# Kernel tuning notes

Measured on AMD Instinct MI355X. Metric: run time of the kernel, lower is better.

The kernel has to match this reference:

```python
import jax, jax.numpy as jnp
import numpy as np

N = 50000   # nodes
E = 800000  # edges (avg degree 16)
D = 96      # feature dim (in = hidden = out)


def setup_inputs() -> dict:
    key = jax.random.key(0)
    ks = jax.random.split(key, 6)
    scale = 1.0 / np.sqrt(D)
    return {
        "x": jax.random.normal(ks[0], (N, D), jnp.float32),
        "edge_index": jax.random.randint(ks[1], (2, E), 0, N, dtype=jnp.int64),
        "W1": jax.random.normal(ks[2], (D, D), jnp.float32) * scale,
        "b1": jnp.zeros((D,), jnp.float32),
        "a1": jnp.full((1,), 0.25, jnp.float32),  # PReLU weight
        "W2": jax.random.normal(ks[3], (D, D), jnp.float32) * scale,
        "b2": jnp.zeros((D,), jnp.float32),
    }


def _gcn_conv(x, W, b, src, dst, norm, n):
    # GCNConv: linear transform, then degree-normalized scatter-add aggregation
    h = x @ W                               # [N, D_out]
    msg = h[src] * norm[:, None]            # gather + scale, [E+N, D_out]
    out = jax.ops.segment_sum(msg, dst, num_segments=n)
    return out + b


def reference(x, edge_index, W1, b1, a1, W2, b2):
    n = x.shape[0]
    # add self loops (PyG gcn_norm default, fill_value=1.0)
    loop = jnp.arange(n, dtype=edge_index.dtype)
    src = jnp.concatenate([edge_index[0], loop])
    dst = jnp.concatenate([edge_index[1], loop])
    # symmetric normalization: D^{-1/2} A D^{-1/2}
    ones = jnp.ones(src.shape[0], dtype=x.dtype)
    deg = jax.ops.segment_sum(ones, dst, num_segments=n)
    dinv = jnp.where(deg > 0, jax.lax.rsqrt(deg), 0.0)
    norm = dinv[src] * dinv[dst]

    h = _gcn_conv(x, W1, b1, src, dst, norm, n)
    h = jnp.where(h > 0, h, a1 * h)  # PReLU (dropout p=0.0 is a no-op)
    h = _gcn_conv(h, W2, b2, src, dst, norm, n)
    return h
```

## Files before the change

### kernel.cpp

```cpp
#include <hip/hip_runtime.h>
#include <hip/hip_bf16.h>

#define NNODES 50000
#define NEDGES 800000
#define DIM    96
#define NBUCK  196
#define CAP    4608
#define TM     64
#define XPAD   104
#define PCH    3125

typedef __attribute__((ext_vector_type(8))) short   short8;
typedef __attribute__((ext_vector_type(4))) float   float4v;

__device__ __forceinline__ float loadF(const void* p, long i, int isbf) {
    return isbf ? __bfloat162float(((const __hip_bfloat16*)p)[i])
                : ((const float*)p)[i];
}
__device__ __forceinline__ int clampN(int v) {
    return v < 0 ? 0 : (v >= NNODES ? NNODES - 1 : v);
}
__device__ __forceinline__ int edgeDst(const int* w, int e, int is64) {
    return clampN(is64 ? w[2 * (NEDGES + e)] : w[NEDGES + e]);
}
__device__ __forceinline__ int edgeSrc(const int* w, int e, int is64) {
    return clampN(is64 ? w[2 * e] : w[e]);
}

__global__ void k_sniff(const unsigned* __restrict__ xw,
                        const unsigned* __restrict__ ew,
                        int* __restrict__ flags,
                        int* __restrict__ bcur) {
    int lane = threadIdx.x;
    for (int i = lane; i < NBUCK; i += 64) bcur[i] = 0;
    int bad = 0, nz = 0;
    for (int r = 0; r < 4; ++r) {
        unsigned w  = xw[lane + 64 * r];
        unsigned lo = w & 0xffffu;
        unsigned ex = (lo >> 7) & 0xffu;
        if (!(lo == 0u || (ex >= 90u && ex <= 145u))) bad++;
        unsigned o = ew[2 * (lane + 64 * r) + 1];
        if (o != 0u) nz++;
    }
    for (int off = 32; off; off >>= 1) {
        bad += __shfl_down(bad, off);
        nz  += __shfl_down(nz,  off);
    }
    if (lane == 0) {
        flags[0] = (bad <= 32) ? 1 : 0;
        flags[1] = (nz  <  4) ? 1 : 0;
    }
}

__global__ __launch_bounds__(256) void k_part(const int* __restrict__ w,
                                              int* __restrict__ bcur,
                                              unsigned* __restrict__ ebuf,
                                              const int* __restrict__ flags) {
    __shared__ unsigned pack[PCH];
    __shared__ int h[NBUCK];
    __shared__ int base[NBUCK];
    const int is64 = flags[1];
    const int tid  = threadIdx.x;
    const int e0   = blockIdx.x * PCH;

    for (int i = tid; i < NBUCK; i += 256) h[i] = 0;
    __syncthreads();
    for (int k = tid; k < PCH; k += 256) {
        int e = e0 + k;
        int s = edgeSrc(w, e, is64);
        int d = edgeDst(w, e, is64);
        pack[k] = ((unsigned)d << 16) | (unsigned)s;
        atomicAdd(&h[d >> 8], 1);
    }
    __syncthreads();
    for (int i = tid; i < NBUCK; i += 256) {
        int c = h[i];
        base[i] = c ? i * CAP + atomicAdd(&bcur[i], c) : 0;
        h[i] = 0;
    }
    __syncthreads();
    for (int k = tid; k < PCH; k += 256) {
        unsigned r = pack[k];
        int b = r >> 24;
        int pos = base[b] + atomicAdd(&h[b], 1);
        if (pos < (b + 1) * CAP) ebuf[pos] = r;
    }
}

__global__ __launch_bounds__(512) void k_csr(const unsigned* __restrict__ ebuf,
                                             const int* __restrict__ bcur,
                                             int* __restrict__ rowbeg,
                                             int* __restrict__ rowend,
                                             unsigned short* __restrict__ col,
                                             float* __restrict__ dinv) {
    __shared__ int h256[256];
    __shared__ int sc[256];
    __shared__ int cur[256];
    const int b   = blockIdx.x;
    const int tid = threadIdx.x;
    int cnt = bcur[b]; if (cnt > CAP) cnt = CAP;
    const int e0 = b * CAP;
    const int e1 = e0 + cnt;

    if (tid < 256) h256[tid] = 0;
    __syncthreads();
    for (int e = e0 + tid; e < e1; e += 512)
        atomicAdd(&h256[(ebuf[e] >> 16) & 255], 1);
    __syncthreads();
    int v = 0;
    if (tid < 256) { v = h256[tid]; sc[tid] = v; }
    __syncthreads();
    for (int off = 1; off < 256; off <<= 1) {
        int t2 = 0;
        if (tid < 256 && tid >= off) t2 = sc[tid - off];
        __syncthreads();
        if (tid < 256) sc[tid] += t2;
        __syncthreads();
    }
    if (tid < 256) {
        int start = e0 + sc[tid] - v;
        cur[tid] = start;
        int node = b * 256 + tid;
        if (node < NNODES) {
            rowbeg[node] = start;
            rowend[node] = start + v;
            dinv[node] = rsqrtf((float)v + 1.0f);
        }
    }
    __syncthreads();
    for (int e = e0 + tid; e < e1; e += 512) {
        unsigned r = ebuf[e];
        int pos = atomicAdd(&cur[(r >> 16) & 255], 1);
        col[pos] = (unsigned short)(r & 0xffffu);
    }
}

__global__ __launch_bounds__(256) void k_gemm_mfma(
        const void* __restrict__ X, int x_force_bf16,
        const void* __restrict__ W,
        const float* __restrict__ dinv,
        __hip_bfloat16* __restrict__ g,
        const int* __restrict__ flags) {
    __shared__ __hip_bfloat16 Xs[TM * XPAD];
    __shared__ __hip_bfloat16 Wt[DIM * XPAD];

    const int t    = threadIdx.x;
    const int fbf  = flags[0];
    const int xbf  = x_force_bf16 ? 1 : fbf;
    const int row0 = blockIdx.x * TM;

    if (!fbf) {
        const float4* Wv = (const float4*)W;
        for (int idx = t; idx < DIM * DIM / 4; idx += 256) {
            int k = idx / (DIM / 4);
            int n = (idx - k * (DIM / 4)) * 4;
            float4 w4 = Wv[idx];
            Wt[(n + 0) * XPAD + k] = __float2bfloat16(w4.x);
            Wt[(n + 1) * XPAD + k] = __float2bfloat16(w4.y);
            Wt[(n + 2) * XPAD + k] = __float2bfloat16(w4.z);
            Wt[(n + 3) * XPAD + k] = __float2bfloat16(w4.w);
        }
    } else {
        for (int idx = t; idx < DIM * DIM; idx += 256) {
            int k = idx / DIM, n = idx - k * DIM;
            Wt[n * XPAD + k] = __float2bfloat16(loadF(W, idx, 1));
        }
    }
    if (!xbf) {
        const float4* Xv = (const float4*)X;
        for (int idx = t; idx < TM * (DIM / 4); idx += 256) {
            int r = idx / (DIM / 4);
            int c = (idx - r * (DIM / 4)) * 4;
            int gr = row0 + r;
            float4 vv = {0.f, 0.f, 0.f, 0.f};
            if (gr < NNODES) vv = Xv[(size_t)gr * (DIM / 4) + (c >> 2)];
            *(__hip_bfloat162*)&Xs[r * XPAD + c] =
                __halves2bfloat162(__float2bfloat16(vv.x), __float2bfloat16(vv.y));
            *(__hip_bfloat162*)&Xs[r * XPAD + c + 2] =
                __halves2bfloat162(__float2bfloat16(vv.z), __float2bfloat16(vv.w));
        }
    } else {
        const short* Xs16 = (const short*)X;
        for (int idx = t; idx < TM * (DIM / 8); idx += 256) {
            int r  = idx / (DIM / 8);
            int c8 = idx - r * (DIM / 8);
            int gr = row0 + r;
            short8 vv = {0, 0, 0, 0, 0, 0, 0, 0};
            if (gr < NNODES) vv = *(const short8*)(Xs16 + (size_t)gr * DIM + c8 * 8);
            *(short8*)((short*)Xs + r * XPAD + c8 * 8) = vv;
        }
    }
    __syncthreads();

    const int wave = t >> 6;
    const int lane = t & 63;
    const int m    = lane & 15;
    const int quad = lane >> 4;

    const short* xsp = (const short*)Xs;
    short8 a[3];
#pragma unroll
    for (int kt = 0; kt < 3; ++kt)
        a[kt] = *(const short8*)(xsp + (wave * 16 + m) * XPAD + kt * 32 + quad * 8);

    float dv[4];
#pragma unroll
    for (int r2 = 0; r2 < 4; ++r2) {
        int gr = row0 + wave * 16 + quad * 4 + r2;
        dv[r2] = (gr < NNODES) ? dinv[gr] : 0.f;
    }

    const short* wtp = (const short*)Wt;
#pragma unroll
    for (int nt = 0; nt < 6; ++nt) {
        float4v acc = {0.f, 0.f, 0.f, 0.f};
#pragma unroll
        for (int kt = 0; kt < 3; ++kt) {
            short8 b = *(const short8*)(wtp + (nt * 16 + m) * XPAD + kt * 32 + quad * 8);
            acc = __builtin_amdgcn_mfma_f32_16x16x32_bf16(a[kt], b, acc, 0, 0, 0);
        }
#pragma unroll
        for (int r2 = 0; r2 < 4; ++r2) {
            int gr = row0 + wave * 16 + quad * 4 + r2;
            if (gr < NNODES)
                g[(size_t)gr * DIM + nt * 16 + m] = __float2bfloat16(acc[r2] * dv[r2]);
        }
    }
}

__global__ __launch_bounds__(256) void k_aggr(
        const __hip_bfloat16* __restrict__ g,
        const int* __restrict__ rowbeg,
        const int* __restrict__ rowend,
        const unsigned short* __restrict__ col,
        const float* __restrict__ dinv,
        const void* __restrict__ b,
        const void* __restrict__ a1,
        void* __restrict__ out,
        const int* __restrict__ flags, int prelu) {
    const int wave = threadIdx.x >> 6;
    const int lane = threadIdx.x & 63;
    const int row  = blockIdx.x * 4 + wave;
    if (row >= NNODES) return;
    const int fbf = flags[0];
    const __hip_bfloat162* gv = (const __hip_bfloat162*)g;
    const int c = lane;

    float2 acc = {0.f, 0.f};
    if (c < 48) acc = __bfloat1622float2(gv[(size_t)row * 48 + c]);

    const int p0 = rowbeg[row], p1 = rowend[row];
    int i = p0;
    for (; i + 16 <= p1; i += 16) {
        int s[16];
#pragma unroll
        for (int k = 0; k < 16; ++k) s[k] = col[i + k];
        if (c < 48) {
            float2 v[16];
#pragma unroll
            for (int k = 0; k < 16; ++k)
                v[k] = __bfloat1622float2(gv[(size_t)s[k] * 48 + c]);
            float2 t0, t1, t2, t3;
            t0.x = (v[0].x + v[1].x) + (v[2].x + v[3].x);
            t0.y = (v[0].y + v[1].y) + (v[2].y + v[3].y);
            t1.x = (v[4].x + v[5].x) + (v[6].x + v[7].x);
            t1.y = (v[4].y + v[5].y) + (v[6].y + v[7].y);
            t2.x = (v[8].x + v[9].x) + (v[10].x + v[11].x);
            t2.y = (v[8].y + v[9].y) + (v[10].y + v[11].y);
            t3.x = (v[12].x + v[13].x) + (v[14].x + v[15].x);
            t3.y = (v[12].y + v[13].y) + (v[14].y + v[15].y);
            acc.x += (t0.x + t1.x) + (t2.x + t3.x);
            acc.y += (t0.y + t1.y) + (t2.y + t3.y);
        }
    }
    for (; i + 8 <= p1; i += 8) {
        int s[8];
#pragma unroll
        for (int k = 0; k < 8; ++k) s[k] = col[i + k];
        if (c < 48) {
            float2 v[8];
#pragma unroll
            for (int k = 0; k < 8; ++k)
                v[k] = __bfloat1622float2(gv[(size_t)s[k] * 48 + c]);
            acc.x += ((v[0].x + v[1].x) + (v[2].x + v[3].x))
                   + ((v[4].x + v[5].x) + (v[6].x + v[7].x));
            acc.y += ((v[0].y + v[1].y) + (v[2].y + v[3].y))
                   + ((v[4].y + v[5].y) + (v[6].y + v[7].y));
        }
    }
    for (; i + 4 <= p1; i += 4) {
        int s0 = col[i], s1 = col[i+1], s2 = col[i+2], s3 = col[i+3];
        if (c < 48) {
            float2 v0 = __bfloat1622float2(gv[(size_t)s0 * 48 + c]);
            float2 v1 = __bfloat1622float2(gv[(size_t)s1 * 48 + c]);
            float2 v2 = __bfloat1622float2(gv[(size_t)s2 * 48 + c]);
            float2 v3 = __bfloat1622float2(gv[(size_t)s3 * 48 + c]);
            acc.x += (v0.x + v1.x) + (v2.x + v3.x);
            acc.y += (v0.y + v1.y) + (v2.y + v3.y);
        }
    }
    for (; i < p1; ++i) {
        int s = col[i];
        if (c < 48) {
            float2 v = __bfloat1622float2(gv[(size_t)s * 48 + c]);
            acc.x += v.x; acc.y += v.y;
        }
    }

    if (c < 48) {
        float dv = dinv[row];
        float vx = dv * acc.x + loadF(b, 2 * c,     fbf);
        float vy = dv * acc.y + loadF(b, 2 * c + 1, fbf);
        if (prelu) {
            float alpha = loadF(a1, 0, fbf);
            vx = vx > 0.f ? vx : alpha * vx;
            vy = vy > 0.f ? vy : alpha * vy;
            ((__hip_bfloat162*)out)[(size_t)row * 48 + c] =
                __halves2bfloat162(__float2bfloat16(vx), __float2bfloat16(vy));
        } else if (fbf) {
            ((__hip_bfloat162*)out)[(size_t)row * 48 + c] =
                __halves2bfloat162(__float2bfloat16(vx), __float2bfloat16(vy));
        } else {
            float2 o; o.x = vx; o.y = vy;
            ((float2*)out)[(size_t)row * 48 + c] = o;
        }
    }
}

extern "C" void kernel_launch(void* const* d_in, const int* in_sizes, int n_in,
                              void* d_out, int out_size, void* d_ws, size_t ws_size,
                              hipStream_t stream) {
    const void* x  = d_in[0];
    const int*  ei = (const int*)d_in[1];
    const void* W1 = d_in[2];
    const void* b1 = d_in[3];
    const void* a1 = d_in[4];
    const void* W2 = d_in[5];
    const void* b2 = d_in[6];

    size_t off = 0;
    auto alloc = [&](size_t bytes) { size_t p = off; off = (off + bytes + 255) & ~(size_t)255; return p; };
    char* ws = (char*)d_ws;
    int*            flags  = (int*)           (ws + alloc(1024));
    float*          dinv   = (float*)         (ws + alloc((size_t)NNODES * 4));
    int*            bcur   = (int*)           (ws + alloc((size_t)NBUCK * 4));
    int*            rowbeg = (int*)           (ws + alloc((size_t)NNODES * 4));
    int*            rowend = (int*)           (ws + alloc((size_t)NNODES * 4));
    unsigned*       ebuf   = (unsigned*)      (ws + alloc((size_t)NBUCK * CAP * 4));
    unsigned short* col    = (unsigned short*)(ws + alloc((size_t)NBUCK * CAP * 2));
    __hip_bfloat16* g      = (__hip_bfloat16*)(ws + alloc((size_t)NNODES * DIM * 2));
    __hip_bfloat16* g2     = (__hip_bfloat16*)(ws + alloc((size_t)NNODES * DIM * 2));
    if (ws_size < off) return;

    k_sniff<<<1, 64, 0, stream>>>((const unsigned*)x, (const unsigned*)ei, flags, bcur);
    k_part <<<256, 256, 0, stream>>>(ei, bcur, ebuf, flags);
    k_csr  <<<NBUCK, 512, 0, stream>>>(ebuf, bcur, rowbeg, rowend, col, dinv);

    const int gemm_grid = (NNODES + TM - 1) / TM;
    const int aggr_grid = (NNODES + 3) / 4;

    k_gemm_mfma<<<gemm_grid, 256, 0, stream>>>(x, 0, W1, dinv, g, flags);
    k_aggr<<<aggr_grid, 256, 0, stream>>>(g, rowbeg, rowend, col, dinv, b1, a1, g2, flags, 1);

    k_gemm_mfma<<<gemm_grid, 256, 0, stream>>>(g2, 1, W2, dinv, g, flags);
    k_aggr<<<aggr_grid, 256, 0, stream>>>(g, rowbeg, rowend, col, dinv, b2, a1, d_out, flags, 0);
}
```

Before: 204.0 us.

## Replace bucketed CSR build with fixed-capacity per-row slots filled by global atomics

The two-pass bucket partition plus per-bucket CSR construction is replaced by a single scatter kernel that atomically bumps each destination's degree and writes the source into a fixed 64-slot row. dinv is recomputed from the degree on the fly, and the aggregation tail loops are merged into one masked 16-wide pass. This removes two kernels and an intermediate edge buffer. In exchange it adds contention on global atomics, makes neighbour order nondeterministic, and silently drops edges beyond 64 per node, which is only safe because random graphs with average degree 16 rarely exceed that.

```diff
diff --git a/kernel.cpp b/kernel.cpp
--- a/kernel.cpp
+++ b/kernel.cpp
@@ -4,11 +4,9 @@
 #define NNODES 50000
 #define NEDGES 800000
 #define DIM    96
-#define NBUCK  196
-#define CAP    4608
+#define RCAP   64
 #define TM     64
 #define XPAD   104
-#define PCH    3125
 
 typedef __attribute__((ext_vector_type(8))) short   short8;
 typedef __attribute__((ext_vector_type(4))) float   float4v;
@@ -20,125 +18,54 @@
 __device__ __forceinline__ int clampN(int v) {
     return v < 0 ? 0 : (v >= NNODES ? NNODES - 1 : v);
 }
-__device__ __forceinline__ int edgeDst(const int* w, int e, int is64) {
-    return clampN(is64 ? w[2 * (NEDGES + e)] : w[NEDGES + e]);
-}
-__device__ __forceinline__ int edgeSrc(const int* w, int e, int is64) {
-    return clampN(is64 ? w[2 * e] : w[e]);
-}
-
-__global__ void k_sniff(const unsigned* __restrict__ xw,
-                        const unsigned* __restrict__ ew,
-                        int* __restrict__ flags,
-                        int* __restrict__ bcur) {
-    int lane = threadIdx.x;
-    for (int i = lane; i < NBUCK; i += 64) bcur[i] = 0;
-    int bad = 0, nz = 0;
-    for (int r = 0; r < 4; ++r) {
-        unsigned w  = xw[lane + 64 * r];
+
+__global__ __launch_bounds__(256) void k_init(const unsigned* __restrict__ xw,
+                                              const unsigned* __restrict__ ew,
+                                              int* __restrict__ flags,
+                                              int* __restrict__ deg) {
+    const int t = blockIdx.x * 256 + threadIdx.x;
+    const int nth = gridDim.x * 256;
+    for (int i = t; i < NNODES; i += nth) deg[i] = 0;
+    if (blockIdx.x == 0) {
+        __shared__ int sn[2];
+        if (threadIdx.x < 2) sn[threadIdx.x] = 0;
+        __syncthreads();
+        unsigned w  = xw[threadIdx.x];
         unsigned lo = w & 0xffffu;
         unsigned ex = (lo >> 7) & 0xffu;
-        if (!(lo == 0u || (ex >= 90u && ex <= 145u))) bad++;
-        unsigned o = ew[2 * (lane + 64 * r) + 1];
-        if (o != 0u) nz++;
-    }
-    for (int off = 32; off; off >>= 1) {
-        bad += __shfl_down(bad, off);
-        nz  += __shfl_down(nz,  off);
-    }
-    if (lane == 0) {
-        flags[0] = (bad <= 32) ? 1 : 0;
-        flags[1] = (nz  <  4) ? 1 : 0;
-    }
-}
-
-__global__ __launch_bounds__(256) void k_part(const int* __restrict__ w,
-                                              int* __restrict__ bcur,
-                                              unsigned* __restrict__ ebuf,
-                                              const int* __restrict__ flags) {
-    __shared__ unsigned pack[PCH];
-    __shared__ int h[NBUCK];
-    __shared__ int base[NBUCK];
-    const int is64 = flags[1];
-    const int tid  = threadIdx.x;
-    const int e0   = blockIdx.x * PCH;
-
-    for (int i = tid; i < NBUCK; i += 256) h[i] = 0;
-    __syncthreads();
-    for (int k = tid; k < PCH; k += 256) {
-        int e = e0 + k;
-        int s = edgeSrc(w, e, is64);
-        int d = edgeDst(w, e, is64);
-        pack[k] = ((unsigned)d << 16) | (unsigned)s;
-        atomicAdd(&h[d >> 8], 1);
-    }
-    __syncthreads();
-    for (int i = tid; i < NBUCK; i += 256) {
-        int c = h[i];
-        base[i] = c ? i * CAP + atomicAdd(&bcur[i], c) : 0;
-        h[i] = 0;
-    }
-    __syncthreads();
-    for (int k = tid; k < PCH; k += 256) {
-        unsigned r = pack[k];
-        int b = r >> 24;
-        int pos = base[b] + atomicAdd(&h[b], 1);
-        if (pos < (b + 1) * CAP) ebuf[pos] = r;
-    }
-}
-
-__global__ __launch_bounds__(512) void k_csr(const unsigned* __restrict__ ebuf,
-                                             const int* __restrict__ bcur,
-                                             int* __restrict__ rowbeg,
-                                             int* __restrict__ rowend,
-                                             unsigned short* __restrict__ col,
-                                             float* __restrict__ dinv) {
-    __shared__ int h256[256];
-    __shared__ int sc[256];
-    __shared__ int cur[256];
-    const int b   = blockIdx.x;
-    const int tid = threadIdx.x;
-    int cnt = bcur[b]; if (cnt > CAP) cnt = CAP;
-    const int e0 = b * CAP;
-    const int e1 = e0 + cnt;
-
-    if (tid < 256) h256[tid] = 0;
-    __syncthreads();
-    for (int e = e0 + tid; e < e1; e += 512)
-        atomicAdd(&h256[(ebuf[e] >> 16) & 255], 1);
-    __syncthreads();
-    int v = 0;
-    if (tid < 256) { v = h256[tid]; sc[tid] = v; }
-    __syncthreads();
-    for (int off = 1; off < 256; off <<= 1) {
-        int t2 = 0;
-        if (tid < 256 && tid >= off) t2 = sc[tid - off];
+        if (!(lo == 0u || (ex >= 90u && ex <= 145u))) atomicAdd(&sn[0], 1);
+        if (ew[2 * threadIdx.x + 1] != 0u) atomicAdd(&sn[1], 1);
         __syncthreads();
-        if (tid < 256) sc[tid] += t2;
-        __syncthreads();
-    }
-    if (tid < 256) {
-        int start = e0 + sc[tid] - v;
-        cur[tid] = start;
-        int node = b * 256 + tid;
-        if (node < NNODES) {
-            rowbeg[node] = start;
-            rowend[node] = start + v;
-            dinv[node] = rsqrtf((float)v + 1.0f);
-        }
-    }
-    __syncthreads();
-    for (int e = e0 + tid; e < e1; e += 512) {
-        unsigned r = ebuf[e];
-        int pos = atomicAdd(&cur[(r >> 16) & 255], 1);
-        col[pos] = (unsigned short)(r & 0xffffu);
-    }
+        if (threadIdx.x == 0) {
+            flags[0] = (sn[0] <= 32) ? 1 : 0;
+            flags[1] = (sn[1] <  4) ? 1 : 0;
+        }
+    }
+}
+
+__global__ __launch_bounds__(256) void k_scatter(const int* __restrict__ w,
+                                                 int* __restrict__ deg,
+                                                 unsigned short* __restrict__ col,
+                                                 const int* __restrict__ flags) {
+    const int e = blockIdx.x * 256 + threadIdx.x;
+    if (e >= NEDGES) return;
+    int s, d;
+    if (flags[1]) {
+        const long* wl = (const long*)w;
+        s = clampN((int)wl[e]);
+        d = clampN((int)wl[NEDGES + e]);
+    } else {
+        s = clampN(w[e]);
+        d = clampN(w[NEDGES + e]);
+    }
+    int pos = atomicAdd(&deg[d], 1);
+    if (pos < RCAP) col[(d << 6) + pos] = (unsigned short)s;
 }
 
 __global__ __launch_bounds__(256) void k_gemm_mfma(
         const void* __restrict__ X, int x_force_bf16,
         const void* __restrict__ W,
-        const float* __restrict__ dinv,
+        const int* __restrict__ deg,
         __hip_bfloat16* __restrict__ g,
         const int* __restrict__ flags) {
     __shared__ __hip_bfloat16 Xs[TM * XPAD];
@@ -207,7 +134,7 @@
 #pragma unroll
     for (int r2 = 0; r2 < 4; ++r2) {
         int gr = row0 + wave * 16 + quad * 4 + r2;
-        dv[r2] = (gr < NNODES) ? dinv[gr] : 0.f;
+        dv[r2] = (gr < NNODES) ? rsqrtf((float)deg[gr] + 1.0f) : 0.f;
     }
 
     const short* wtp = (const short*)Wt;
@@ -230,10 +157,8 @@
 
 __global__ __launch_bounds__(256) void k_aggr(
         const __hip_bfloat16* __restrict__ g,
-        const int* __restrict__ rowbeg,
-        const int* __restrict__ rowend,
+        const int* __restrict__ deg,
         const unsigned short* __restrict__ col,
-        const float* __restrict__ dinv,
         const void* __restrict__ b,
         const void* __restrict__ a1,
         void* __restrict__ out,
@@ -249,7 +174,10 @@
     float2 acc = {0.f, 0.f};
     if (c < 48) acc = __bfloat1622float2(gv[(size_t)row * 48 + c]);
 
-    const int p0 = rowbeg[row], p1 = rowend[row];
+    const int dg = deg[row];
+    const int nn = dg < RCAP ? dg : RCAP;
+    const int p0 = row << 6;
+    const int p1 = p0 + nn;
     int i = p0;
     for (; i + 16 <= p1; i += 16) {
         int s[16];
@@ -273,42 +201,37 @@
             acc.y += (t0.y + t1.y) + (t2.y + t3.y);
         }
     }
-    for (; i + 8 <= p1; i += 8) {
-        int s[8];
-#pragma unroll
-        for (int k = 0; k < 8; ++k) s[k] = col[i + k];
+    if (i < p1) {
+        const int last = p1 - 1;
+        int s[16];
+#pragma unroll
+        for (int k = 0; k < 16; ++k) {
+            int idx = i + k;
+            s[k] = col[idx > last ? last : idx];
+        }
         if (c < 48) {
-            float2 v[8];
-#pragma unroll
-            for (int k = 0; k < 8; ++k)
+            float2 v[16];
+#pragma unroll
+            for (int k = 0; k < 16; ++k) {
                 v[k] = __bfloat1622float2(gv[(size_t)s[k] * 48 + c]);
-            acc.x += ((v[0].x + v[1].x) + (v[2].x + v[3].x))
-                   + ((v[4].x + v[5].x) + (v[6].x + v[7].x));
-            acc.y += ((v[0].y + v[1].y) + (v[2].y + v[3].y))
-                   + ((v[4].y + v[5].y) + (v[6].y + v[7].y));
-        }
-    }
-    for (; i + 4 <= p1; i += 4) {
-        int s0 = col[i], s1 = col[i+1], s2 = col[i+2], s3 = col[i+3];
-        if (c < 48) {
-            float2 v0 = __bfloat1622float2(gv[(size_t)s0 * 48 + c]);
-            float2 v1 = __bfloat1622float2(gv[(size_t)s1 * 48 + c]);
-            float2 v2 = __bfloat1622float2(gv[(size_t)s2 * 48 + c]);
-            float2 v3 = __bfloat1622float2(gv[(size_t)s3 * 48 + c]);
-            acc.x += (v0.x + v1.x) + (v2.x + v3.x);
-            acc.y += (v0.y + v1.y) + (v2.y + v3.y);
-        }
-    }
-    for (; i < p1; ++i) {
-        int s = col[i];
-        if (c < 48) {
-            float2 v = __bfloat1622float2(gv[(size_t)s * 48 + c]);
-            acc.x += v.x; acc.y += v.y;
+                if (i + k > last) { v[k].x = 0.f; v[k].y = 0.f; }
+            }
+            float2 t0, t1, t2, t3;
+            t0.x = (v[0].x + v[1].x) + (v[2].x + v[3].x);
+            t0.y = (v[0].y + v[1].y) + (v[2].y + v[3].y);
+            t1.x = (v[4].x + v[5].x) + (v[6].x + v[7].x);
+            t1.y = (v[4].y + v[5].y) + (v[6].y + v[7].y);
+            t2.x = (v[8].x + v[9].x) + (v[10].x + v[11].x);
+            t2.y = (v[8].y + v[9].y) + (v[10].y + v[11].y);
+            t3.x = (v[12].x + v[13].x) + (v[14].x + v[15].x);
+            t3.y = (v[12].y + v[13].y) + (v[14].y + v[15].y);
+            acc.x += (t0.x + t1.x) + (t2.x + t3.x);
+            acc.y += (t0.y + t1.y) + (t2.y + t3.y);
         }
     }
 
     if (c < 48) {
-        float dv = dinv[row];
+        float dv = rsqrtf((float)dg + 1.0f);
         float vx = dv * acc.x + loadF(b, 2 * c,     fbf);
         float vy = dv * acc.y + loadF(b, 2 * c + 1, fbf);
         if (prelu) {
@@ -341,27 +264,22 @@
     size_t off = 0;
     auto alloc = [&](size_t bytes) { size_t p = off; off = (off + bytes + 255) & ~(size_t)255; return p; };
     char* ws = (char*)d_ws;
-    int*            flags  = (int*)           (ws + alloc(1024));
-    float*          dinv   = (float*)         (ws + alloc((size_t)NNODES * 4));
-    int*            bcur   = (int*)           (ws + alloc((size_t)NBUCK * 4));
-    int*            rowbeg = (int*)           (ws + alloc((size_t)NNODES * 4));
-    int*            rowend = (int*)           (ws + alloc((size_t)NNODES * 4));
-    unsigned*       ebuf   = (unsigned*)      (ws + alloc((size_t)NBUCK * CAP * 4));
-    unsigned short* col    = (unsigned short*)(ws + alloc((size_t)NBUCK * CAP * 2));
-    __hip_bfloat16* g      = (__hip_bfloat16*)(ws + alloc((size_t)NNODES * DIM * 2));
-    __hip_bfloat16* g2     = (__hip_bfloat16*)(ws + alloc((size_t)NNODES * DIM * 2));
+    int*            flags = (int*)           (ws + alloc(1024));
+    int*            deg   = (int*)           (ws + alloc((size_t)NNODES * 4));
+    unsigned short* col   = (unsigned short*)(ws + alloc((size_t)NNODES * RCAP * 2));
+    __hip_bfloat16* g     = (__hip_bfloat16*)(ws + alloc((size_t)NNODES * DIM * 2));
+    __hip_bfloat16* g2    = (__hip_bfloat16*)(ws + alloc((size_t)NNODES * DIM * 2));
     if (ws_size < off) return;
 
-    k_sniff<<<1, 64, 0, stream>>>((const unsigned*)x, (const unsigned*)ei, flags, bcur);
-    k_part <<<256, 256, 0, stream>>>(ei, bcur, ebuf, flags);
-    k_csr  <<<NBUCK, 512, 0, stream>>>(ebuf, bcur, rowbeg, rowend, col, dinv);
+    k_init   <<<128, 256, 0, stream>>>((const unsigned*)x, (const unsigned*)ei, flags, deg);
+    k_scatter<<<(NEDGES + 255) / 256, 256, 0, stream>>>(ei, deg, col, flags);
 
     const int gemm_grid = (NNODES + TM - 1) / TM;
     const int aggr_grid = (NNODES + 3) / 4;
 
-    k_gemm_mfma<<<gemm_grid, 256, 0, stream>>>(x, 0, W1, dinv, g, flags);
-    k_aggr<<<aggr_grid, 256, 0, stream>>>(g, rowbeg, rowend, col, dinv, b1, a1, g2, flags, 1);
-
-    k_gemm_mfma<<<gemm_grid, 256, 0, stream>>>(g2, 1, W2, dinv, g, flags);
-    k_aggr<<<aggr_grid, 256, 0, stream>>>(g, rowbeg, rowend, col, dinv, b2, a1, d_out, flags, 0);
-}
+    k_gemm_mfma<<<gemm_grid, 256, 0, stream>>>(x, 0, W1, deg, g, flags);
+    k_aggr<<<aggr_grid, 256, 0, stream>>>(g, deg, col, b1, a1, g2, flags, 1);
+
+    k_gemm_mfma<<<gemm_grid, 256, 0, stream>>>(g2, 1, W2, deg, g, flags);
+    k_aggr<<<aggr_grid, 256, 0, stream>>>(g, deg, col, b2, a1, d_out, flags, 0);
+}
```

Result: slower. 215.7 us (+5.7%).

## Aggregate two rows per wave with 8-byte vector gathers in SpMM

Applied to the files above, without the earlier changes.

The aggregation kernel now assigns two destination rows to each wavefront, with 24 lanes per row each loading 4 bf16 values (uint2) instead of 48 lanes loading 2. This raises lane utilisation from 48 of 64 to 48 of 64 across two rows, and halves the number of gather instructions per neighbour. Neighbour loops run to the max degree of the pair, using clamped indices and masking, which wastes work when the two degrees differ. The col buffer gets padding and the grid is halved to match.

```diff
diff --git a/kernel.cpp b/kernel.cpp
--- a/kernel.cpp
+++ b/kernel.cpp
@@ -25,6 +25,14 @@
 }
 __device__ __forceinline__ int edgeSrc(const int* w, int e, int is64) {
     return clampN(is64 ? w[2 * e] : w[e]);
+}
+__device__ __forceinline__ float4 unpack4(uint2 r) {
+    __hip_bfloat162 lo = *(__hip_bfloat162*)&r.x;
+    __hip_bfloat162 hi = *(__hip_bfloat162*)&r.y;
+    float2 l2 = __bfloat1622float2(lo);
+    float2 h2 = __bfloat1622float2(hi);
+    float4 o; o.x = l2.x; o.y = l2.y; o.z = h2.x; o.w = h2.y;
+    return o;
 }
 
 __global__ void k_sniff(const unsigned* __restrict__ xw,
@@ -240,89 +248,85 @@
         const int* __restrict__ flags, int prelu) {
     const int wave = threadIdx.x >> 6;
     const int lane = threadIdx.x & 63;
-    const int row  = blockIdx.x * 4 + wave;
-    if (row >= NNODES) return;
-    const int fbf = flags[0];
-    const __hip_bfloat162* gv = (const __hip_bfloat162*)g;
-    const int c = lane;
-
-    float2 acc = {0.f, 0.f};
-    if (c < 48) acc = __bfloat1622float2(gv[(size_t)row * 48 + c]);
-
-    const int p0 = rowbeg[row], p1 = rowend[row];
-    int i = p0;
-    for (; i + 16 <= p1; i += 16) {
-        int s[16];
-#pragma unroll
-        for (int k = 0; k < 16; ++k) s[k] = col[i + k];
-        if (c < 48) {
-            float2 v[16];
-#pragma unroll
-            for (int k = 0; k < 16; ++k)
-                v[k] = __bfloat1622float2(gv[(size_t)s[k] * 48 + c]);
-            float2 t0, t1, t2, t3;
+    const int rowA = blockIdx.x * 8 + wave * 2;
+    if (rowA >= NNODES) return;
+    const int rowB  = rowA + 1;
+    const int hasB  = rowB < NNODES;
+    const int half  = lane >= 24;
+    const int sub   = half ? lane - 24 : lane;
+    const bool act  = (lane < 48) && (!half || hasB);
+    const int myrow = half ? rowB : rowA;
+    const int fbf   = flags[0];
+
+    const uint2* gv2 = (const uint2*)g;
+
+    float4 acc = {0.f, 0.f, 0.f, 0.f};
+    if (act) acc = unpack4(gv2[(size_t)myrow * 24 + sub]);
+
+    const int pA0 = rowbeg[rowA];
+    const int degA = rowend[rowA] - pA0;
+    int pB0 = pA0, degB = 0;
+    if (hasB) { pB0 = rowbeg[rowB]; degB = rowend[rowB] - pB0; }
+    const int pM0  = half ? pB0 : pA0;
+    const int degM = half ? degB : degA;
+    const int maxd = degA > degB ? degA : degB;
+
+    for (int j0 = 0; j0 < maxd; j0 += 8) {
+        int sA[8], sB[8];
+#pragma unroll
+        for (int k = 0; k < 8; ++k) {
+            int jA = j0 + k; jA = jA >= degA ? degA - 1 : jA; jA = jA < 0 ? 0 : jA;
+            int jB = j0 + k; jB = jB >= degB ? degB - 1 : jB; jB = jB < 0 ? 0 : jB;
+            sA[k] = col[pA0 + jA];
+            sB[k] = hasB ? col[pB0 + jB] : 0;
+        }
+        if (act) {
+            float4 v[8];
+#pragma unroll
+            for (int k = 0; k < 8; ++k) {
+                int s = half ? sB[k] : sA[k];
+                v[k] = unpack4(gv2[(size_t)s * 24 + sub]);
+                if (j0 + k >= degM) { v[k].x = 0.f; v[k].y = 0.f; v[k].z = 0.f; v[k].w = 0.f; }
+            }
+            float4 t0, t1;
             t0.x = (v[0].x + v[1].x) + (v[2].x + v[3].x);
             t0.y = (v[0].y + v[1].y) + (v[2].y + v[3].y);
+            t0.z = (v[0].z + v[1].z) + (v[2].z + v[3].z);
+            t0.w = (v[0].w + v[1].w) + (v[2].w + v[3].w);
             t1.x = (v[4].x + v[5].x) + (v[6].x + v[7].x);
             t1.y = (v[4].y + v[5].y) + (v[6].y + v[7].y);
-            t2.x = (v[8].x + v[9].x) + (v[10].x + v[11].x);
-            t2.y = (v[8].y + v[9].y) + (v[10].y + v[11].y);
-            t3.x = (v[12].x + v[13].x) + (v[14].x + v[15].x);
-            t3.y = (v[12].y + v[13].y) + (v[14].y + v[15].y);
-            acc.x += (t0.x + t1.x) + (t2.x + t3.x);
-            acc.y += (t0.y + t1.y) + (t2.y + t3.y);
-        }
-    }
-    for (; i + 8 <= p1; i += 8) {
-        int s[8];
-#pragma unroll
-        for (int k = 0; k < 8; ++k) s[k] = col[i + k];
-        if (c < 48) {
-            float2 v[8];
-#pragma unroll
-            for (int k = 0; k < 8; ++k)
-                v[k] = __bfloat1622float2(gv[(size_t)s[k] * 48 + c]);
-            acc.x += ((v[0].x + v[1].x) + (v[2].x + v[3].x))
-                   + ((v[4].x + v[5].x) + (v[6].x + v[7].x));
-            acc.y += ((v[0].y + v[1].y) + (v[2].y + v[3].y))
-                   + ((v[4].y + v[5].y) + (v[6].y + v[7].y));
-        }
-    }
-    for (; i + 4 <= p1; i += 4) {
-        int s0 = col[i], s1 = col[i+1], s2 = col[i+2], s3 = col[i+3];
-        if (c < 48) {
-            float2 v0 = __bfloat1622float2(gv[(size_t)s0 * 48 + c]);
-            float2 v1 = __bfloat1622float2(gv[(size_t)s1 * 48 + c]);
-            float2 v2 = __bfloat1622float2(gv[(size_t)s2 * 48 + c]);
-            float2 v3 = __bfloat1622float2(gv[(size_t)s3 * 48 + c]);
-            acc.x += (v0.x + v1.x) + (v2.x + v3.x);
-            acc.y += (v0.y + v1.y) + (v2.y + v3.y);
-        }
-    }
-    for (; i < p1; ++i) {
-        int s = col[i];
-        if (c < 48) {
-            float2 v = __bfloat1622float2(gv[(size_t)s * 48 + c]);
-            acc.x += v.x; acc.y += v.y;
-        }
-    }
-
-    if (c < 48) {
-        float dv = dinv[row];
-        float vx = dv * acc.x + loadF(b, 2 * c,     fbf);
-        float vy = dv * acc.y + loadF(b, 2 * c + 1, fbf);
+            t1.z = (v[4].z + v[5].z) + (v[6].z + v[7].z);
+            t1.w = (v[4].w + v[5].w) + (v[6].w + v[7].w);
+            acc.x += t0.x + t1.x;
+            acc.y += t0.y + t1.y;
+            acc.z += t0.z + t1.z;
+            acc.w += t0.w + t1.w;
+        }
+    }
+    (void)pM0;
+
+    if (act) {
+        float dv = dinv[myrow];
+        float v0 = dv * acc.x + loadF(b, 4 * sub,     fbf);
+        float v1 = dv * acc.y + loadF(b, 4 * sub + 1, fbf);
+        float v2 = dv * acc.z + loadF(b, 4 * sub + 2, fbf);
+        float v3 = dv * acc.w + loadF(b, 4 * sub + 3, fbf);
         if (prelu) {
             float alpha = loadF(a1, 0, fbf);
-            vx = vx > 0.f ? vx : alpha * vx;
-            vy = vy > 0.f ? vy : alpha * vy;
-            ((__hip_bfloat162*)out)[(size_t)row * 48 + c] =
-                __halves2bfloat162(__float2bfloat16(vx), __float2bfloat16(vy));
-        } else if (fbf) {
-            ((__hip_bfloat162*)out)[(size_t)row * 48 + c] =
-                __halves2bfloat162(__float2bfloat16(vx), __float2bfloat16(vy));
+            v0 = v0 > 0.f ? v0 : alpha * v0;
+            v1 = v1 > 0.f ? v1 : alpha * v1;
+            v2 = v2 > 0.f ? v2 : alpha * v2;
+            v3 = v3 > 0.f ? v3 : alpha * v3;
+        }
+        if (prelu || fbf) {
+            uint2 o;
+            __hip_bfloat162 lo = __halves2bfloat162(__float2bfloat16(v0), __float2bfloat16(v1));
+            __hip_bfloat162 hi = __halves2bfloat162(__float2bfloat16(v2), __float2bfloat16(v3));
+            o.x = *(unsigned*)&lo; o.y = *(unsigned*)&hi;
+            ((uint2*)out)[(size_t)myrow * 24 + sub] = o;
         } else {
-            float2 o; o.x = vx; o.y = vy;
-            ((float2*)out)[(size_t)row * 48 + c] = o;
+            float4 o; o.x = v0; o.y = v1; o.z = v2; o.w = v3;
+            ((float4*)out)[(size_t)myrow * 24 + sub] = o;
         }
     }
 }
@@ -347,7 +351,7 @@
     int*            rowbeg = (int*)           (ws + alloc((size_t)NNODES * 4));
     int*            rowend = (int*)           (ws + alloc((size_t)NNODES * 4));
     unsigned*       ebuf   = (unsigned*)      (ws + alloc((size_t)NBUCK * CAP * 4));
-    unsigned short* col    = (unsigned short*)(ws + alloc((size_t)NBUCK * CAP * 2));
+    unsigned short* col    = (unsigned short*)(ws + alloc((size_t)NBUCK * CAP * 2 + 256));
     __hip_bfloat16* g      = (__hip_bfloat16*)(ws + alloc((size_t)NNODES * DIM * 2));
     __hip_bfloat16* g2     = (__hip_bfloat16*)(ws + alloc((size_t)NNODES * DIM * 2));
     if (ws_size < off) return;
@@ -357,7 +361,7 @@
     k_csr  <<<NBUCK, 512, 0, stream>>>(ebuf, bcur, rowbeg, rowend, col, dinv);
 
     const int gemm_grid = (NNODES + TM - 1) / TM;
-    const int aggr_grid = (NNODES + 3) / 4;
+    const int aggr_grid = (NNODES + 7) / 8;
 
     k_gemm_mfma<<<gemm_grid, 256, 0, stream>>>(x, 0, W1, dinv, g, flags);
     k_aggr<<<aggr_grid, 256, 0, stream>>>(g, rowbeg, rowend, col, dinv, b1, a1, g2, flags, 1);
```

New measurement: 230.7 us. +13.1%, slower.

## Aggregate per feature column from LDS-staged transposed features with split CSR

Applied to the files above, without the earlier changes.

Node features are now stored feature-major (transposed) after the GEMM. Aggregation runs one block per feature column and row chunk, staging half of that column (about 50 KB of bf16) in shared memory. The CSR columns are split by source half so each row's neighbours are gathered from LDS rather than from random global rows. A final transpose kernel restores row-major output. This removes scattered global gathers but rereads the column list once per feature (96 times) and adds a transpose kernel plus extra staging traffic.

```diff
diff --git a/kernel.cpp b/kernel.cpp
--- a/kernel.cpp
+++ b/kernel.cpp
@@ -9,8 +9,14 @@
 #define TM     64
 #define XPAD   104
 #define PCH    3125
+#define GTS    50048
+#define GHALF  25024
+#define ARC    5
+#define ACH    10000
+#define ARPT   20
 
 typedef __attribute__((ext_vector_type(8))) short   short8;
+typedef __attribute__((ext_vector_type(4))) short   short4v;
 typedef __attribute__((ext_vector_type(4))) float   float4v;
 
 __device__ __forceinline__ float loadF(const void* p, long i, int isbf) {
@@ -25,6 +31,14 @@
 }
 __device__ __forceinline__ int edgeSrc(const int* w, int e, int is64) {
     return clampN(is64 ? w[2 * e] : w[e]);
+}
+__device__ __forceinline__ float bfbits2f(unsigned short u) {
+    unsigned x = ((unsigned)u) << 16;
+    return __uint_as_float(x);
+}
+__device__ __forceinline__ unsigned short f2bfbits(float f) {
+    __hip_bfloat16 h = __float2bfloat16(f);
+    return *(unsigned short*)&h;
 }
 
 __global__ void k_sniff(const unsigned* __restrict__ xw,
@@ -90,12 +104,14 @@
 __global__ __launch_bounds__(512) void k_csr(const unsigned* __restrict__ ebuf,
                                              const int* __restrict__ bcur,
                                              int* __restrict__ rowbeg,
+                                             int* __restrict__ rowmid,
                                              int* __restrict__ rowend,
                                              unsigned short* __restrict__ col,
                                              float* __restrict__ dinv) {
     __shared__ int h256[256];
     __shared__ int sc[256];
-    __shared__ int cur[256];
+    __shared__ int cur_lo[256];
+    __shared__ int cur_hi[256];
     const int b   = blockIdx.x;
     const int tid = threadIdx.x;
     int cnt = bcur[b]; if (cnt > CAP) cnt = CAP;
@@ -119,7 +135,8 @@
     }
     if (tid < 256) {
         int start = e0 + sc[tid] - v;
-        cur[tid] = start;
+        cur_lo[tid] = start;
+        cur_hi[tid] = start + v - 1;
         int node = b * 256 + tid;
         if (node < NNODES) {
             rowbeg[node] = start;
@@ -130,23 +147,30 @@
     __syncthreads();
     for (int e = e0 + tid; e < e1; e += 512) {
         unsigned r = ebuf[e];
-        int pos = atomicAdd(&cur[(r >> 16) & 255], 1);
-        col[pos] = (unsigned short)(r & 0xffffu);
+        int dl = (r >> 16) & 255;
+        int s  = (int)(r & 0xffffu);
+        int pos = (s < GHALF) ? atomicAdd(&cur_lo[dl], 1)
+                              : atomicAdd(&cur_hi[dl], -1);
+        col[pos] = (unsigned short)s;
+    }
+    __syncthreads();
+    if (tid < 256) {
+        int node = b * 256 + tid;
+        if (node < NNODES) rowmid[node] = cur_lo[tid];
     }
 }
 
 __global__ __launch_bounds__(256) void k_gemm_mfma(
-        const void* __restrict__ X, int x_force_bf16,
+        const void* __restrict__ X, int xmode,
         const void* __restrict__ W,
         const float* __restrict__ dinv,
-        __hip_bfloat16* __restrict__ g,
+        unsigned short* __restrict__ gt,
         const int* __restrict__ flags) {
     __shared__ __hip_bfloat16 Xs[TM * XPAD];
     __shared__ __hip_bfloat16 Wt[DIM * XPAD];
 
     const int t    = threadIdx.x;
     const int fbf  = flags[0];
-    const int xbf  = x_force_bf16 ? 1 : fbf;
     const int row0 = blockIdx.x * TM;
 
     if (!fbf) {
@@ -166,7 +190,19 @@
             Wt[n * XPAD + k] = __float2bfloat16(loadF(W, idx, 1));
         }
     }
-    if (!xbf) {
+    if (xmode == 1) {
+        const unsigned short* ht = (const unsigned short*)X;
+        short* xs = (short*)Xs;
+        for (int idx = t; idx < DIM * 16; idx += 256) {
+            int c  = idx >> 4;
+            int sg = idx & 15;
+            short4v v = *(const short4v*)(ht + (size_t)c * GTS + row0 + sg * 4);
+            xs[(sg * 4 + 0) * XPAD + c] = v[0];
+            xs[(sg * 4 + 1) * XPAD + c] = v[1];
+            xs[(sg * 4 + 2) * XPAD + c] = v[2];
+            xs[(sg * 4 + 3) * XPAD + c] = v[3];
+        }
+    } else if (!fbf) {
         const float4* Xv = (const float4*)X;
         for (int idx = t; idx < TM * (DIM / 4); idx += 256) {
             int r = idx / (DIM / 4);
@@ -203,12 +239,11 @@
     for (int kt = 0; kt < 3; ++kt)
         a[kt] = *(const short8*)(xsp + (wave * 16 + m) * XPAD + kt * 32 + quad * 8);
 
+    const int gr0 = row0 + wave * 16 + quad * 4;
     float dv[4];
 #pragma unroll
-    for (int r2 = 0; r2 < 4; ++r2) {
-        int gr = row0 + wave * 16 + quad * 4 + r2;
-        dv[r2] = (gr < NNODES) ? dinv[gr] : 0.f;
-    }
+    for (int r2 = 0; r2 < 4; ++r2)
+        dv[r2] = (gr0 + r2 < NNODES) ? dinv[gr0 + r2] : 0.f;
 
     const short* wtp = (const short*)Wt;
 #pragma unroll
@@ -219,110 +254,171 @@
             short8 b = *(const short8*)(wtp + (nt * 16 + m) * XPAD + kt * 32 + quad * 8);
             acc = __builtin_amdgcn_mfma_f32_16x16x32_bf16(a[kt], b, acc, 0, 0, 0);
         }
-#pragma unroll
-        for (int r2 = 0; r2 < 4; ++r2) {
-            int gr = row0 + wave * 16 + quad * 4 + r2;
-            if (gr < NNODES)
-                g[(size_t)gr * DIM + nt * 16 + m] = __float2bfloat16(acc[r2] * dv[r2]);
-        }
-    }
-}
-
-__global__ __launch_bounds__(256) void k_aggr(
-        const __hip_bfloat16* __restrict__ g,
+        short4v o;
+        o[0] = (short)f2bfbits(acc[0] * dv[0]);
+        o[1] = (short)f2bfbits(acc[1] * dv[1]);
+        o[2] = (short)f2bfbits(acc[2] * dv[2]);
+        o[3] = (short)f2bfbits(acc[3] * dv[3]);
+        *(short4v*)(gt + (size_t)(nt * 16 + m) * GTS + gr0) = o;
+    }
+}
+
+__device__ __forceinline__ float gather8(const unsigned short* __restrict__ cb,
+                                         const unsigned short* __restrict__ col,
+                                         int j, int last, int sub) {
+    int i0 = j     > last ? last : j;
+    int i1 = j + 1 > last ? last : j + 1;
+    int i2 = j + 2 > last ? last : j + 2;
+    int i3 = j + 3 > last ? last : j + 3;
+    int i4 = j + 4 > last ? last : j + 4;
+    int i5 = j + 5 > last ? last : j + 5;
+    int i6 = j + 6 > last ? last : j + 6;
+    int i7 = j + 7 > last ? last : j + 7;
+    int s0 = col[i0] - sub, s1 = col[i1] - sub, s2 = col[i2] - sub, s3 = col[i3] - sub;
+    int s4 = col[i4] - sub, s5 = col[i5] - sub, s6 = col[i6] - sub, s7 = col[i7] - sub;
+    float v0 = (j     <= last) ? bfbits2f(cb[s0]) : 0.f;
+    float v1 = (j + 1 <= last) ? bfbits2f(cb[s1]) : 0.f;
+    float v2 = (j + 2 <= last) ? bfbits2f(cb[s2]) : 0.f;
+    float v3 = (j + 3 <= last) ? bfbits2f(cb[s3]) : 0.f;
+    float v4 = (j + 4 <= last) ? bfbits2f(cb[s4]) : 0.f;
+    float v5 = (j + 5 <= last) ? bfbits2f(cb[s5]) : 0.f;
+    float v6 = (j + 6 <= last) ? bfbits2f(cb[s6]) : 0.f;
+    float v7 = (j + 7 <= last) ? bfbits2f(cb[s7]) : 0.f;
+    return ((v0 + v1) + (v2 + v3)) + ((v4 + v5) + (v6 + v7));
+}
+
+__global__ __launch_bounds__(512, 4) void k_aggr_t(
+        const unsigned short* __restrict__ gt,
         const int* __restrict__ rowbeg,
+        const int* __restrict__ rowmid,
         const int* __restrict__ rowend,
         const unsigned short* __restrict__ col,
         const float* __restrict__ dinv,
         const void* __restrict__ b,
         const void* __restrict__ a1,
-        void* __restrict__ out,
+        void* __restrict__ outt,
         const int* __restrict__ flags, int prelu) {
-    const int wave = threadIdx.x >> 6;
-    const int lane = threadIdx.x & 63;
-    const int row  = blockIdx.x * 4 + wave;
-    if (row >= NNODES) return;
+    __shared__ unsigned short cb[GHALF];
+    const int tid   = threadIdx.x;
+    const int c     = blockIdx.x % DIM;
+    const int rbase = (blockIdx.x / DIM) * ACH;
+    const int fbf   = flags[0];
+    const size_t cg = (size_t)c * GTS;
+
+    float acc[ARPT];
+#pragma unroll
+    for (int r = 0; r < ARPT; ++r) acc[r] = 0.f;
+
+    {
+        const uint4* src = (const uint4*)(gt + cg);
+        for (int i = tid; i < GHALF / 8; i += 512) ((uint4*)cb)[i] = src[i];
+    }
+    __syncthreads();
+#pragma unroll
+    for (int r = 0; r < ARPT; ++r) {
+        if (tid + r * 512 < ACH) {
+            int row = rbase + tid + r * 512;
+            int j = rowbeg[row], je = rowmid[row];
+            float a = 0.f;
+            while (j + 8 <= je) { a += gather8(cb, col, j, je - 1, 0); j += 8; }
+            if (j < je)          a += gather8(cb, col, j, je - 1, 0);
+            if (row < GHALF) a += bfbits2f(cb[row]);
+            acc[r] += a;
+        }
+    }
+    __syncthreads();
+    {
+        const uint4* src = (const uint4*)(gt + cg + GHALF);
+        for (int i = tid; i < GHALF / 8; i += 512) ((uint4*)cb)[i] = src[i];
+    }
+    __syncthreads();
+#pragma unroll
+    for (int r = 0; r < ARPT; ++r) {
+        if (tid + r * 512 < ACH) {
+            int row = rbase + tid + r * 512;
+            int j = rowmid[row], je = rowend[row];
+            float a = 0.f;
+            while (j + 8 <= je) { a += gather8(cb, col, j, je - 1, GHALF); j += 8; }
+            if (j < je)          a += gather8(cb, col, j, je - 1, GHALF);
+            if (row >= GHALF) a += bfbits2f(cb[row - GHALF]);
+            acc[r] += a;
+        }
+    }
+
+    const float bias  = loadF(b, c, fbf);
+    const float alpha = prelu ? loadF(a1, 0, fbf) : 0.f;
+#pragma unroll
+    for (int r = 0; r < ARPT; ++r) {
+        if (tid + r * 512 < ACH) {
+            int row = rbase + tid + r * 512;
+            float v = dinv[row] * acc[r] + bias;
+            if (prelu) v = v > 0.f ? v : alpha * v;
+            if (prelu || fbf)
+                ((unsigned short*)outt)[cg + row] = f2bfbits(v);
+            else
+                ((float*)outt)[cg + row] = v;
+        }
+    }
+}
+
+__global__ __launch_bounds__(256) void k_trans(const void* __restrict__ ot,
+                                               void* __restrict__ out,
+                                               const int* __restrict__ flags) {
+    __shared__ __align__(16) char tbuf[DIM * 66 * 4];
     const int fbf = flags[0];
-    const __hip_bfloat162* gv = (const __hip_bfloat162*)g;
-    const int c = lane;
-
-    float2 acc = {0.f, 0.f};
-    if (c < 48) acc = __bfloat1622float2(gv[(size_t)row * 48 + c]);
-
-    const int p0 = rowbeg[row], p1 = rowend[row];
-    int i = p0;
-    for (; i + 16 <= p1; i += 16) {
-        int s[16];
-#pragma unroll
-        for (int k = 0; k < 16; ++k) s[k] = col[i + k];
-        if (c < 48) {
-            float2 v[16];
-#pragma unroll
-            for (int k = 0; k < 16; ++k)
-                v[k] = __bfloat1622float2(gv[(size_t)s[k] * 48 + c]);
-            float2 t0, t1, t2, t3;
-            t0.x = (v[0].x + v[1].x) + (v[2].x + v[3].x);
-            t0.y = (v[0].y + v[1].y) + (v[2].y + v[3].y);
-            t1.x = (v[4].x + v[5].x) + (v[6].x + v[7].x);
-            t1.y = (v[4].y + v[5].y) + (v[6].y + v[7].y);
-            t2.x = (v[8].x + v[9].x) + (v[10].x + v[11].x);
-            t2.y = (v[8].y + v[9].y) + (v[10].y + v[11].y);
-            t3.x = (v[12].x + v[13].x) + (v[14].x + v[15].x);
-            t3.y = (v[12].y + v[13].y) + (v[14].y + v[15].y);
-            acc.x += (t0.x + t1.x) + (t2.x + t3.x);
-            acc.y += (t0.y + t1.y) + (t2.y + t3.y);
-        }
-    }
-    for (; i + 8 <= p1; i += 8) {
-        int s[8];
-#pragma unroll
-        for (int k = 0; k < 8; ++k) s[k] = col[i + k];
-        if (c < 48) {
-            float2 v[8];
-#pragma unroll
-            for (int k = 0; k < 8; ++k)
-                v[k] = __bfloat1622float2(gv[(size_t)s[k] * 48 + c]);
-            acc.x += ((v[0].x + v[1].x) + (v[2].x + v[3].x))
-                   + ((v[4].x + v[5].x) + (v[6].x + v[7].x));
-            acc.y += ((v[0].y + v[1].y) + (v[2].y + v[3].y))
-                   + ((v[4].y + v[5].y) + (v[6].y + v[7].y));
-        }
-    }
-    for (; i + 4 <= p1; i += 4) {
-        int s0 = col[i], s1 = col[i+1], s2 = col[i+2], s3 = col[i+3];
-        if (c < 48) {
-            float2 v0 = __bfloat1622float2(gv[(size_t)s0 * 48 + c]);
-            float2 v1 = __bfloat1622float2(gv[(size_t)s1 * 48 + c]);
-            float2 v2 = __bfloat1622float2(gv[(size_t)s2 * 48 + c]);
-            float2 v3 = __bfloat1622float2(gv[(size_t)s3 * 48 + c]);
-            acc.x += (v0.x + v1.x) + (v2.x + v3.x);
-            acc.y += (v0.y + v1.y) + (v2.y + v3.y);
-        }
-    }
-    for (; i < p1; ++i) {
-        int s = col[i];
-        if (c < 48) {
-            float2 v = __bfloat1622float2(gv[(size_t)s * 48 + c]);
-            acc.x += v.x; acc.y += v.y;
-        }
-    }
-
-    if (c < 48) {
-        float dv = dinv[row];
-        float vx = dv * acc.x + loadF(b, 2 * c,     fbf);
-        float vy = dv * acc.y + loadF(b, 2 * c + 1, fbf);
-        if (prelu) {
-            float alpha = loadF(a1, 0, fbf);
-            vx = vx > 0.f ? vx : alpha * vx;
-            vy = vy > 0.f ? vy : alpha * vy;
-            ((__hip_bfloat162*)out)[(size_t)row * 48 + c] =
-                __halves2bfloat162(__float2bfloat16(vx), __float2bfloat16(vy));
-        } else if (fbf) {
-            ((__hip_bfloat162*)out)[(size_t)row * 48 + c] =
-                __halves2bfloat162(__float2bfloat16(vx), __float2bfloat16(vy));
-        } else {
-            float2 o; o.x = vx; o.y = vy;
-            ((float2*)out)[(size_t)row * 48 + c] = o;
+    const int t   = threadIdx.x;
+    const int r0  = blockIdx.x * 64;
+    const int r   = t >> 2;
+    const int q   = t & 3;
+
+    if (fbf) {
+        unsigned short (*tile)[68] = (unsigned short(*)[68])tbuf;
+        const unsigned short* src = (const unsigned short*)ot;
+        for (int idx = t; idx < DIM * 16; idx += 256) {
+            int c = idx >> 4, sg = idx & 15;
+            short4v v = *(const short4v*)(src + (size_t)c * GTS + r0 + sg * 4);
+            tile[c][sg * 4 + 0] = (unsigned short)v[0];
+            tile[c][sg * 4 + 1] = (unsigned short)v[1];
+            tile[c][sg * 4 + 2] = (unsigned short)v[2];
+            tile[c][sg * 4 + 3] = (unsigned short)v[3];
+        }
+        __syncthreads();
+        if (r0 + r < NNODES) {
+            short8 w0, w1, w2;
+#pragma unroll
+            for (int k = 0; k < 8; ++k) {
+                w0[k] = (short)tile[q * 24 + k][r];
+                w1[k] = (short)tile[q * 24 + 8 + k][r];
+                w2[k] = (short)tile[q * 24 + 16 + k][r];
+            }
+            unsigned short* dst = (unsigned short*)out + (size_t)(r0 + r) * DIM + q * 24;
+            *(short8*)(dst)      = w0;
+            *(short8*)(dst + 8)  = w1;
+            *(short8*)(dst + 16) = w2;
+        }
+    } else {
+        float (*tf)[66] = (float(*)[66])tbuf;
+        const float* src = (const float*)ot;
+        for (int idx = t; idx < DIM * 16; idx += 256) {
+            int c = idx >> 4, sg = idx & 15;
+            float4 v = *(const float4*)(src + (size_t)c * GTS + r0 + sg * 4);
+            tf[c][sg * 4 + 0] = v.x;
+            tf[c][sg * 4 + 1] = v.y;
+            tf[c][sg * 4 + 2] = v.z;
+            tf[c][sg * 4 + 3] = v.w;
+        }
+        __syncthreads();
+        if (r0 + r < NNODES) {
+            float* dst = (float*)out + (size_t)(r0 + r) * DIM + q * 24;
+#pragma unroll
+            for (int k6 = 0; k6 < 6; ++k6) {
+                float4 v;
+                v.x = tf[q * 24 + k6 * 4 + 0][r];
+                v.y = tf[q * 24 + k6 * 4 + 1][r];
+                v.z = tf[q * 24 + k6 * 4 + 2][r];
+                v.w = tf[q * 24 + k6 * 4 + 3][r];
+                *(float4*)(dst + k6 * 4) = v;
+            }
         }
     }
 }
@@ -345,23 +441,27 @@
     float*          dinv   = (float*)         (ws + alloc((size_t)NNODES * 4));
     int*            bcur   = (int*)           (ws + alloc((size_t)NBUCK * 4));
     int*            rowbeg = (int*)           (ws + alloc((size_t)NNODES * 4));
+    int*            rowmid = (int*)           (ws + alloc((size_t)NNODES * 4));
     int*            rowend = (int*)           (ws + alloc((size_t)NNODES * 4));
     unsigned*       ebuf   = (unsigned*)      (ws + alloc((size_t)NBUCK * CAP * 4));
-    unsigned short* col    = (unsigned short*)(ws + alloc((size_t)NBUCK * CAP * 2));
-    __hip_bfloat16* g      = (__hip_bfloat16*)(ws + alloc((size_t)NNODES * DIM * 2));
-    __hip_bfloat16* g2     = (__hip_bfloat16*)(ws + alloc((size_t)NNODES * DIM * 2));
+    unsigned short* col    = (unsigned short*)(ws + alloc((size_t)NBUCK * CAP * 2 + 256));
+    unsigned short* gt     = (unsigned short*)(ws + alloc((size_t)DIM * GTS * 2));
+    unsigned short* ht     = (unsigned short*)(ws + alloc((size_t)DIM * GTS * 2));
+    void*           ot     = (void*)          (ws + alloc((size_t)DIM * GTS * 4));
     if (ws_size < off) return;
 
     k_sniff<<<1, 64, 0, stream>>>((const unsigned*)x, (const unsigned*)ei, flags, bcur);
     k_part <<<256, 256, 0, stream>>>(ei, bcur, ebuf, flags);
-    k_csr  <<<NBUCK, 512, 0, stream>>>(ebuf, bcur, rowbeg, rowend, col, dinv);
+    k_csr  <<<NBUCK, 512, 0, stream>>>(ebuf, bcur, rowbeg, rowmid, rowend, col, dinv);
 
     const int gemm_grid = (NNODES + TM - 1) / TM;
-    const int aggr_grid = (NNODES + 3) / 4;
-
-    k_gemm_mfma<<<gemm_grid, 256, 0, stream>>>(x, 0, W1, dinv, g, flags);
-    k_aggr<<<aggr_grid, 256, 0, stream>>>(g, rowbeg, rowend, col, dinv, b1, a1, g2, flags, 1);
-
-    k_gemm_mfma<<<gemm_grid, 256, 0, stream>>>(g2, 1, W2, dinv, g, flags);
-    k_aggr<<<aggr_grid, 256, 0, stream>>>(g, rowbeg, rowend, col, dinv, b2, a1, d_out, flags, 0);
-}
+    const int aggr_grid = DIM * ARC;
+
+    k_gemm_mfma<<<gemm_grid, 256, 0, stream>>>(x, 0, W1, dinv, gt, flags);
+    k_aggr_t<<<aggr_grid, 512, 0, stream>>>(gt, rowbeg, rowmid, rowend, col,
+                                            dinv, b1, a1, ht, flags, 1);
+    k_gemm_mfma<<<gemm_grid, 256, 0, stream>>>(ht, 1, W2, dinv, gt, flags);
+    k_aggr_t<<<aggr_grid, 512, 0, stream>>>(gt, rowbeg, rowmid, rowend, col,
+                                            dinv, b2, a1, ot, flags, 0);
+    k_trans<<<gemm_grid, 256, 0, stream>>>(ot, d_out, flags);
+}
```

New measurement: 317.7 us. 55.7% more time.
